# Kernel optimization log

Measured on AMD Instinct MI355X. Metric: run time of the kernel, lower is better.

The kernel has to match this reference:

```python
import jax, jax.numpy as jnp
import numpy as np

N = 100000      # nodes
E = 800000      # edges (avg degree 8)
D_IN = 64
H1 = H2 = H3 = 64
HEADS = 2
D_EDGE = 5
NEG_SLOPE = 0.2  # GATConv leaky_relu slope


def _lin(key, fi, fo):
    kw, kb = jax.random.split(key)
    w = jax.random.normal(kw, (fi, fo), jnp.float32) / np.sqrt(fi)
    b = jax.random.normal(kb, (fo,), jnp.float32) * 0.01
    return w, b


def setup_inputs() -> dict:
    key = jax.random.key(0)
    ks = jax.random.split(key, 16)
    x = jax.random.normal(ks[0], (N, D_IN), jnp.float32)
    edge_index = jax.random.randint(ks[1], (2, E), 0, N, dtype=jnp.int32)
    edge_attr = jax.random.normal(ks[2], (E, D_EDGE), jnp.float32)

    inp = {"x": x, "edge_index": edge_index, "edge_attr": edge_attr}
    dims = [(D_IN, H1), (H1, H2), (H2, H3)]
    for i, (fi, fo) in enumerate(dims, start=1):
        k = jax.random.fold_in(ks[3], i)
        ka, kb, kc = jax.random.split(k, 3)
        inp[f"w_node{i}"], inp[f"b_node{i}"] = _lin(ka, fi, fo)
        inp[f"w_edge{i}"], inp[f"b_edge{i}"] = _lin(kb, D_EDGE, fo)
        inp[f"w_comb{i}"], inp[f"b_comb{i}"] = _lin(kc, 2 * fo, fo)
    # GATConv: shared lin for src/dst, att vectors, bias (concat=False -> size H3)
    kg, ks_, kd, kbias = jax.random.split(ks[4], 4)
    inp["w_gat"] = jax.random.normal(kg, (H3, HEADS * H3), jnp.float32) / np.sqrt(H3)
    inp["att_src"] = jax.random.normal(ks_, (HEADS, H3), jnp.float32) * 0.1
    inp["att_dst"] = jax.random.normal(kd, (HEADS, H3), jnp.float32) * 0.1
    inp["b_gat"] = jax.random.normal(kbias, (H3,), jnp.float32) * 0.01
    return inp


def _edge_conv(h, src, dst, ea, wn, bn, we, be, wc, bc, n):
    # lin_node / lin_edge applied densely, then gather -> concat -> lin -> scatter-add
    hn = h @ wn + bn                       # [N, C]
    ef = ea @ we + be                      # [E, C]
    msg = jnp.concatenate([hn[src], ef], axis=1) @ wc + bc  # [E, C]
    return jax.ops.segment_sum(msg, dst, num_segments=n)


def _gat(h, src, dst, w_gat, att_src, att_dst, b_gat, n):
    g = (h @ w_gat).reshape(n, HEADS, -1)          # [N, H, C]
    a_src = jnp.einsum("nhc,hc->nh", g, att_src)    # [N, H]
    a_dst = jnp.einsum("nhc,hc->nh", g, att_dst)
    alpha = jax.nn.leaky_relu(a_src[src] + a_dst[dst], NEG_SLOPE)  # [E, H]
    # segment softmax over incoming edges of each dst node
    m = jax.ops.segment_max(alpha, dst, num_segments=n)
    alpha = jnp.exp(alpha - m[dst])
    denom = jax.ops.segment_sum(alpha, dst, num_segments=n)
    alpha = alpha / (denom[dst] + 1e-16)
    out = jax.ops.segment_sum(g[src] * alpha[:, :, None], dst, num_segments=n)  # [N,H,C]
    return out.mean(axis=1) + b_gat  # concat=False -> mean over heads, plus bias


def reference(x, edge_index, edge_attr,
              w_node1, b_node1, w_edge1, b_edge1, w_comb1, b_comb1,
              w_node2, b_node2, w_edge2, b_edge2, w_comb2, b_comb2,
              w_node3, b_node3, w_edge3, b_edge3, w_comb3, b_comb3,
              w_gat, att_src, att_dst, b_gat):
    n = x.shape[0]
    src, dst = edge_index[0], edge_index[1]
    h = x
    h = jax.nn.relu(_edge_conv(h, src, dst, edge_attr, w_node1, b_node1, w_edge1, b_edge1, w_comb1, b_comb1, n))
    h = jax.nn.relu(_edge_conv(h, src, dst, edge_attr, w_node2, b_node2, w_edge2, b_edge2, w_comb2, b_comb2, n))
    h = jax.nn.relu(_edge_conv(h, src, dst, edge_attr, w_node3, b_node3, w_edge3, b_edge3, w_comb3, b_comb3, n))
    h = _gat(h, src, dst, w_gat, att_src, att_dst, b_gat, n)
    return h.reshape(-1)  # torch.flatten
```

## Files before the change

kernel.cpp:

```cpp
#include <hip/hip_runtime.h>
#include <hip/hip_fp16.h>
#include <math.h>


#define TPB 256

typedef unsigned int u32;

__device__ inline float2 f16unpack2(u32 u) {
    __half2 h = *reinterpret_cast<__half2*>(&u);
    return __half22float2(h);
}
__device__ inline u32 f16pack2(float lo, float hi) {
    __half2 h = __floats2half2_rn(lo, hi);
    return *reinterpret_cast<u32*>(&h);
}
__device__ inline void fma_f16x8(float* acc, uint4 v, float w) {
    float2 t;
    t = f16unpack2(v.x); acc[0] = fmaf(w, t.x, acc[0]); acc[1] = fmaf(w, t.y, acc[1]);
    t = f16unpack2(v.y); acc[2] = fmaf(w, t.x, acc[2]); acc[3] = fmaf(w, t.y, acc[3]);
    t = f16unpack2(v.z); acc[4] = fmaf(w, t.x, acc[4]); acc[5] = fmaf(w, t.y, acc[5]);
    t = f16unpack2(v.w); acc[6] = fmaf(w, t.x, acc[6]); acc[7] = fmaf(w, t.y, acc[7]);
}
__device__ inline void acc_h16(float4& acc, uint2 v) {
    float2 a = f16unpack2(v.x);
    float2 b = f16unpack2(v.y);
    acc.x += a.x; acc.y += a.y; acc.z += b.x; acc.w += b.y;
}

#define MAC4(acc, a, w0, w1, w2, w3)                                           \
    acc.x = fmaf(a.x, w0.x, acc.x); acc.y = fmaf(a.x, w0.y, acc.y);            \
    acc.z = fmaf(a.x, w0.z, acc.z); acc.w = fmaf(a.x, w0.w, acc.w);            \
    acc.x = fmaf(a.y, w1.x, acc.x); acc.y = fmaf(a.y, w1.y, acc.y);            \
    acc.z = fmaf(a.y, w1.z, acc.z); acc.w = fmaf(a.y, w1.w, acc.w);            \
    acc.x = fmaf(a.z, w2.x, acc.x); acc.y = fmaf(a.z, w2.y, acc.y);            \
    acc.z = fmaf(a.z, w2.z, acc.z); acc.w = fmaf(a.z, w2.w, acc.w);            \
    acc.x = fmaf(a.w, w3.x, acc.x); acc.y = fmaf(a.w, w3.y, acc.y);            \
    acc.z = fmaf(a.w, w3.z, acc.z); acc.w = fmaf(a.w, w3.w, acc.w);

__global__ __launch_bounds__(TPB) void k_hist(const int* __restrict__ dst, int* __restrict__ cnt,
                                              int* __restrict__ rank, int E) {
    int e = blockIdx.x * TPB + threadIdx.x;
    if (e < E) rank[e] = atomicAdd(&cnt[dst[e]], 1);
}

__global__ __launch_bounds__(TPB) void k_scan1(int* __restrict__ data, int* __restrict__ partials, int n) {
    __shared__ int s[TPB];
    int i = blockIdx.x * TPB + threadIdx.x;
    int v = (i < n) ? data[i] : 0;
    s[threadIdx.x] = v;
    __syncthreads();
    for (int off = 1; off < TPB; off <<= 1) {
        int t = (threadIdx.x >= off) ? s[threadIdx.x - off] : 0;
        __syncthreads();
        s[threadIdx.x] += t;
        __syncthreads();
    }
    if (i < n) data[i] = s[threadIdx.x] - v;
    if (threadIdx.x == TPB - 1) partials[blockIdx.x] = s[TPB - 1];
}

__global__ __launch_bounds__(1024) void k_scan2(int* __restrict__ partials, int nb) {
    __shared__ int s[1024];
    int v = (threadIdx.x < nb) ? partials[threadIdx.x] : 0;
    s[threadIdx.x] = v;
    __syncthreads();
    for (int off = 1; off < 1024; off <<= 1) {
        int t = (threadIdx.x >= off) ? s[threadIdx.x - off] : 0;
        __syncthreads();
        s[threadIdx.x] += t;
        __syncthreads();
    }
    if (threadIdx.x < nb) partials[threadIdx.x] = s[threadIdx.x] - v;
}

__global__ __launch_bounds__(TPB) void k_scan3(int* __restrict__ data, const int* __restrict__ partials,
                                               int n, int total) {
    int i = blockIdx.x * TPB + threadIdx.x;
    if (i < n) data[i] += partials[blockIdx.x];
    if (i == 0) data[n] = total;
}

__global__ __launch_bounds__(TPB) void k_scatter(const int* __restrict__ src, const int* __restrict__ dst,
                                                 const int* __restrict__ rank, const int* __restrict__ row_start,
                                                 int2* __restrict__ csr_se, int E) {
    int e = blockIdx.x * TPB + threadIdx.x;
    if (e < E) {
        int idx = row_start[dst[e]] + rank[e];
        csr_se[idx] = make_int2(src[e], e);
    }
}

__global__ __launch_bounds__(TPB) void k_aggB5(const int2* __restrict__ csr_se, const int* __restrict__ row_start,
                                               const float* __restrict__ EA, float* __restrict__ B5, int n) {
    const int node = blockIdx.x * 16 + (threadIdx.x >> 4);
    if (node >= n) return;
    const int lid = threadIdx.x & 15;
    const int beg = row_start[node], end = row_start[node + 1];
    float b0 = 0.f, b1 = 0.f, b2 = 0.f, b3 = 0.f, b4 = 0.f;
    for (int j = beg + lid; j < end; j += 16) {
        int e = csr_se[j].y;
        const float* p = EA + (size_t)e * 5;
        b0 += p[0]; b1 += p[1]; b2 += p[2]; b3 += p[3]; b4 += p[4];
    }
    #pragma unroll
    for (int off = 1; off < 16; off <<= 1) {
        b0 += __shfl_xor(b0, off); b1 += __shfl_xor(b1, off);
        b2 += __shfl_xor(b2, off); b3 += __shfl_xor(b3, off);
        b4 += __shfl_xor(b4, off);
    }
    if (lid == 0) {
        float* bp = B5 + (size_t)node * 5;
        bp[0] = b0; bp[1] = b1; bp[2] = b2; bp[3] = b3; bp[4] = b4;
    }
}

struct CombPtrs {
    const float* wn; const float* bn;
    const float* we; const float* be;
    const float* wc; const float* bc;
    float* W1;
};

__global__ __launch_bounds__(TPB) void k_combine3(CombPtrs p0, CombPtrs p1, CombPtrs p2) {
    CombPtrs P = (blockIdx.x == 0) ? p0 : ((blockIdx.x == 1) ? p1 : p2);
    const float* wn = P.wn; const float* bn = P.bn;
    const float* we = P.we; const float* be = P.be;
    const float* wc = P.wc; const float* bc = P.bc;
    float* W1 = P.W1;
    float* W2 = P.W1 + 4096;
    float* cv = P.W1 + 4416;
    int tid = threadIdx.x;
    for (int idx = tid; idx < 64 * 64; idx += TPB) {
        int i = idx >> 6, j = idx & 63;
        float acc = 0.f;
        #pragma unroll 8
        for (int k = 0; k < 64; k++) acc = fmaf(wn[i * 64 + k], wc[k * 64 + j], acc);
        W1[idx] = acc;
    }
    for (int idx = tid; idx < 5 * 64; idx += TPB) {
        int i = idx >> 6, j = idx & 63;
        float acc = 0.f;
        #pragma unroll 8
        for (int k = 0; k < 64; k++) acc = fmaf(we[i * 64 + k], wc[(64 + k) * 64 + j], acc);
        W2[idx] = acc;
    }
    for (int j = tid; j < 64; j += TPB) {
        float acc = bc[j];
        for (int k = 0; k < 64; k++) {
            acc = fmaf(bn[k], wc[k * 64 + j], acc);
            acc = fmaf(be[k], wc[(64 + k) * 64 + j], acc);
        }
        cv[j] = acc;
    }
}

template <bool IN16, bool OUT16>
__global__ __launch_bounds__(TPB, 6) void k_ec_fused(const void* __restrict__ Hv,
                                                     const int* __restrict__ row_start,
                                                     const int2* __restrict__ csr_se,
                                                     const float* __restrict__ Wfold,
                                                     const float* __restrict__ B5,
                                                     void* __restrict__ OUTv, int n) {
    __shared__ float Alds[64 * 68];
    const float* Hf = (const float*)Hv;
    const u32*   Hh = (const u32*)Hv;
    const int t = threadIdx.x;
    const int base = blockIdx.x * 64;

    const int lane = t & 63;
    const int lid = lane & 15;
    const int gbase = lane & 48;
    const int gid = t >> 4;
    const int c4 = lid * 4;
    const int h2i = lid * 2;
    for (int i = 0; i < 4; i++) {
        int r = gid * 4 + i;
        int node = base + r;
        float4 acc = make_float4(0.f, 0.f, 0.f, 0.f);
        if (node < n) {
            int beg = row_start[node], end = row_start[node + 1];
            for (int chunk = beg; chunk < end; chunk += 16) {
                int cdeg = min(end - chunk, 16);
                int s_l = (chunk + lid < end) ? csr_se[chunk + lid].x : 0;
                int it = 0;
                for (; it + 7 < cdeg; it += 8) {
                    int se0 = __shfl(s_l, gbase + it);
                    int se1 = __shfl(s_l, gbase + it + 1);
                    int se2 = __shfl(s_l, gbase + it + 2);
                    int se3 = __shfl(s_l, gbase + it + 3);
                    int se4 = __shfl(s_l, gbase + it + 4);
                    int se5 = __shfl(s_l, gbase + it + 5);
                    int se6 = __shfl(s_l, gbase + it + 6);
                    int se7 = __shfl(s_l, gbase + it + 7);
                    if (IN16) {
                        uint2 v0 = *(const uint2*)&Hh[(size_t)se0 * 32 + h2i];
                        uint2 v1 = *(const uint2*)&Hh[(size_t)se1 * 32 + h2i];
                        uint2 v2 = *(const uint2*)&Hh[(size_t)se2 * 32 + h2i];
                        uint2 v3 = *(const uint2*)&Hh[(size_t)se3 * 32 + h2i];
                        uint2 v4 = *(const uint2*)&Hh[(size_t)se4 * 32 + h2i];
                        uint2 v5 = *(const uint2*)&Hh[(size_t)se5 * 32 + h2i];
                        uint2 v6 = *(const uint2*)&Hh[(size_t)se6 * 32 + h2i];
                        uint2 v7 = *(const uint2*)&Hh[(size_t)se7 * 32 + h2i];
                        acc_h16(acc, v0); acc_h16(acc, v1); acc_h16(acc, v2); acc_h16(acc, v3);
                        acc_h16(acc, v4); acc_h16(acc, v5); acc_h16(acc, v6); acc_h16(acc, v7);
                    } else {
                        float4 v0 = *(const float4*)&Hf[(size_t)se0 * 64 + c4];
                        float4 v1 = *(const float4*)&Hf[(size_t)se1 * 64 + c4];
                        float4 v2 = *(const float4*)&Hf[(size_t)se2 * 64 + c4];
                        float4 v3 = *(const float4*)&Hf[(size_t)se3 * 64 + c4];
                        float4 v4 = *(const float4*)&Hf[(size_t)se4 * 64 + c4];
                        float4 v5 = *(const float4*)&Hf[(size_t)se5 * 64 + c4];
                        float4 v6 = *(const float4*)&Hf[(size_t)se6 * 64 + c4];
                        float4 v7 = *(const float4*)&Hf[(size_t)se7 * 64 + c4];
                        acc.x += ((v0.x + v1.x) + (v2.x + v3.x)) + ((v4.x + v5.x) + (v6.x + v7.x));
                        acc.y += ((v0.y + v1.y) + (v2.y + v3.y)) + ((v4.y + v5.y) + (v6.y + v7.y));
                        acc.z += ((v0.z + v1.z) + (v2.z + v3.z)) + ((v4.z + v5.z) + (v6.z + v7.z));
                        acc.w += ((v0.w + v1.w) + (v2.w + v3.w)) + ((v4.w + v5.w) + (v6.w + v7.w));
                    }
                }
                for (; it + 3 < cdeg; it += 4) {
                    int se0 = __shfl(s_l, gbase + it);
                    int se1 = __shfl(s_l, gbase + it + 1);
                    int se2 = __shfl(s_l, gbase + it + 2);
                    int se3 = __shfl(s_l, gbase + it + 3);
                    if (IN16) {
                        uint2 v0 = *(const uint2*)&Hh[(size_t)se0 * 32 + h2i];
                        uint2 v1 = *(const uint2*)&Hh[(size_t)se1 * 32 + h2i];
                        uint2 v2 = *(const uint2*)&Hh[(size_t)se2 * 32 + h2i];
                        uint2 v3 = *(const uint2*)&Hh[(size_t)se3 * 32 + h2i];
                        acc_h16(acc, v0); acc_h16(acc, v1); acc_h16(acc, v2); acc_h16(acc, v3);
                    } else {
                        float4 v0 = *(const float4*)&Hf[(size_t)se0 * 64 + c4];
                        float4 v1 = *(const float4*)&Hf[(size_t)se1 * 64 + c4];
                        float4 v2 = *(const float4*)&Hf[(size_t)se2 * 64 + c4];
                        float4 v3 = *(const float4*)&Hf[(size_t)se3 * 64 + c4];
                        acc.x += (v0.x + v1.x) + (v2.x + v3.x);
                        acc.y += (v0.y + v1.y) + (v2.y + v3.y);
                        acc.z += (v0.z + v1.z) + (v2.z + v3.z);
                        acc.w += (v0.w + v1.w) + (v2.w + v3.w);
                    }
                }
                for (; it < cdeg; it++) {
                    int se = __shfl(s_l, gbase + it);
                    if (IN16) {
                        uint2 v = *(const uint2*)&Hh[(size_t)se * 32 + h2i];
                        acc_h16(acc, v);
                    } else {
                        float4 v = *(const float4*)&Hf[(size_t)se * 64 + c4];
                        acc.x += v.x; acc.y += v.y; acc.z += v.z; acc.w += v.w;
                    }
                }
            }
        }
        *(float4*)&Alds[r * 68 + c4] = acc;
    }
    __syncthreads();

    const int r0 = (t >> 4) * 4, c0 = (t & 15) * 4;
    float4 acc0 = make_float4(0.f, 0.f, 0.f, 0.f), acc1 = acc0, acc2 = acc0, acc3 = acc0;
    #pragma unroll 2
    for (int k = 0; k < 64; k += 4) {
        float4 a0 = *(float4*)&Alds[(r0 + 0) * 68 + k];
        float4 a1 = *(float4*)&Alds[(r0 + 1) * 68 + k];
        float4 a2 = *(float4*)&Alds[(r0 + 2) * 68 + k];
        float4 a3 = *(float4*)&Alds[(r0 + 3) * 68 + k];
        float4 w0 = *(const float4*)&Wfold[(k + 0) * 64 + c0];
        float4 w1 = *(const float4*)&Wfold[(k + 1) * 64 + c0];
        float4 w2 = *(const float4*)&Wfold[(k + 2) * 64 + c0];
        float4 w3 = *(const float4*)&Wfold[(k + 3) * 64 + c0];
        MAC4(acc0, a0, w0, w1, w2, w3);
        MAC4(acc1, a1, w0, w1, w2, w3);
        MAC4(acc2, a2, w0, w1, w2, w3);
        MAC4(acc3, a3, w0, w1, w2, w3);
    }
    float4 w2c[5];
    #pragma unroll
    for (int j = 0; j < 5; j++) w2c[j] = *(const float4*)&Wfold[4096 + j * 64 + c0];
    const float4 cv4 = *(const float4*)&Wfold[4416 + c0];
    #define EC_STORE(i, acc)                                                        \
        { int row = base + r0 + i;                                                  \
          if (row < n) {                                                            \
              const float* bp = B5 + (size_t)row * 5;                               \
              float deg = (float)(row_start[row + 1] - row_start[row]);             \
              float4 q;                                                             \
              q.x = deg * cv4.x; q.y = deg * cv4.y;                                 \
              q.z = deg * cv4.z; q.w = deg * cv4.w;                                 \
              for (int j = 0; j < 5; j++) {                                         \
                  float b = bp[j];                                                  \
                  q.x = fmaf(b, w2c[j].x, q.x); q.y = fmaf(b, w2c[j].y, q.y);       \
                  q.z = fmaf(b, w2c[j].z, q.z); q.w = fmaf(b, w2c[j].w, q.w);       \
              }                                                                     \
              float4 r4;                                                            \
              r4.x = fmaxf(acc.x + q.x, 0.f); r4.y = fmaxf(acc.y + q.y, 0.f);       \
              r4.z = fmaxf(acc.z + q.z, 0.f); r4.w = fmaxf(acc.w + q.w, 0.f);       \
              if (OUT16) {                                                          \
                  u32* O = (u32*)OUTv;                                              \
                  uint2 g;                                                          \
                  g.x = f16pack2(r4.x, r4.y); g.y = f16pack2(r4.z, r4.w);           \
                  *(uint2*)&O[(size_t)row * 32 + (c0 >> 1)] = g;                    \
              } else {                                                              \
                  float* O = (float*)OUTv;                                          \
                  *(float4*)&O[(size_t)row * 64 + c0] = r4;                         \
              } } }
    EC_STORE(0, acc0) EC_STORE(1, acc1) EC_STORE(2, acc2) EC_STORE(3, acc3)
    #undef EC_STORE
}

__global__ __launch_bounds__(TPB) void k_gemm_gat(const u32* __restrict__ Hh, const float* __restrict__ W,
                                                  const float* __restrict__ att_src, const float* __restrict__ att_dst,
                                                  u32* __restrict__ Gh, float* __restrict__ asrc,
                                                  float* __restrict__ adst, int n) {
    __shared__ float Alds[64 * 68];
    __shared__ float Wlds[64 * 132];
    const int t = threadIdx.x;
    const int base = blockIdx.x * 64;
    {
        int r16 = t >> 4, cc = (t & 15) * 4;
        #pragma unroll
        for (int rep = 0; rep < 4; rep++) {
            int r = rep * 16 + r16;
            int row = base + r;
            float4 v = make_float4(0.f, 0.f, 0.f, 0.f);
            if (row < n) {
                uint2 h = *(const uint2*)&Hh[(size_t)row * 32 + (cc >> 1)];
                float2 a = f16unpack2(h.x), b = f16unpack2(h.y);
                v = make_float4(a.x, a.y, b.x, b.y);
            }
            *(float4*)&Alds[r * 68 + cc] = v;
        }
        #pragma unroll
        for (int rep = 0; rep < 8; rep++) {
            int idx4 = (rep * 256 + t) * 4;
            int r = idx4 >> 7, c = idx4 & 127;
            *(float4*)&Wlds[r * 132 + c] = *(const float4*)&W[r * 128 + c];
        }
    }
    __syncthreads();

    const int r0 = (t >> 4) * 4, c0 = (t & 15) * 4;
    float4 p00 = make_float4(0.f, 0.f, 0.f, 0.f), p01 = p00, p02 = p00, p03 = p00;
    float4 p10 = p00, p11 = p00, p12 = p00, p13 = p00;
    #pragma unroll 2
    for (int k = 0; k < 64; k += 4) {
        float4 a0 = *(float4*)&Alds[(r0 + 0) * 68 + k];
        float4 a1 = *(float4*)&Alds[(r0 + 1) * 68 + k];
        float4 a2 = *(float4*)&Alds[(r0 + 2) * 68 + k];
        float4 a3 = *(float4*)&Alds[(r0 + 3) * 68 + k];
        float4 u0 = *(float4*)&Wlds[(k + 0) * 132 + c0];
        float4 u1 = *(float4*)&Wlds[(k + 1) * 132 + c0];
        float4 u2 = *(float4*)&Wlds[(k + 2) * 132 + c0];
        float4 u3 = *(float4*)&Wlds[(k + 3) * 132 + c0];
        MAC4(p00, a0, u0, u1, u2, u3);
        MAC4(p01, a1, u0, u1, u2, u3);
        MAC4(p02, a2, u0, u1, u2, u3);
        MAC4(p03, a3, u0, u1, u2, u3);
        float4 v0 = *(float4*)&Wlds[(k + 0) * 132 + 64 + c0];
        float4 v1 = *(float4*)&Wlds[(k + 1) * 132 + 64 + c0];
        float4 v2 = *(float4*)&Wlds[(k + 2) * 132 + 64 + c0];
        float4 v3 = *(float4*)&Wlds[(k + 3) * 132 + 64 + c0];
        MAC4(p10, a0, v0, v1, v2, v3);
        MAC4(p11, a1, v0, v1, v2, v3);
        MAC4(p12, a2, v0, v1, v2, v3);
        MAC4(p13, a3, v0, v1, v2, v3);
    }
    const float4 as0 = *(const float4*)&att_src[c0];
    const float4 as1 = *(const float4*)&att_src[64 + c0];
    const float4 ad0 = *(const float4*)&att_dst[c0];
    const float4 ad1 = *(const float4*)&att_dst[64 + c0];
    #define DOT4(a, b) (a.x * b.x + a.y * b.y + a.z * b.z + a.w * b.w)
    #define GAT_ROW(i, h0, h1)                                                      \
        { int row = base + r0 + i;                                                  \
          float s0 = DOT4(h0, as0), s1 = DOT4(h1, as1);                             \
          float d0 = DOT4(h0, ad0), d1 = DOT4(h1, ad1);                             \
          s0 += __shfl_xor(s0, 1); s1 += __shfl_xor(s1, 1);                         \
          d0 += __shfl_xor(d0, 1); d1 += __shfl_xor(d1, 1);                         \
          s0 += __shfl_xor(s0, 2); s1 += __shfl_xor(s1, 2);                         \
          d0 += __shfl_xor(d0, 2); d1 += __shfl_xor(d1, 2);                         \
          s0 += __shfl_xor(s0, 4); s1 += __shfl_xor(s1, 4);                         \
          d0 += __shfl_xor(d0, 4); d1 += __shfl_xor(d1, 4);                         \
          s0 += __shfl_xor(s0, 8); s1 += __shfl_xor(s1, 8);                         \
          d0 += __shfl_xor(d0, 8); d1 += __shfl_xor(d1, 8);                         \
          if (row < n) {                                                            \
              uint2 g0; g0.x = f16pack2(h0.x, h0.y); g0.y = f16pack2(h0.z, h0.w);   \
              uint2 g1; g1.x = f16pack2(h1.x, h1.y); g1.y = f16pack2(h1.z, h1.w);   \
              *(uint2*)&Gh[(size_t)row * 64 + (c0 >> 1)] = g0;                      \
              *(uint2*)&Gh[(size_t)row * 64 + 32 + (c0 >> 1)] = g1;                 \
              if ((t & 15) == 0) {                                                  \
                  float2 sv; sv.x = s0; sv.y = s1;                                  \
                  float2 dv; dv.x = d0; dv.y = d1;                                  \
                  *(float2*)&asrc[(size_t)row * 2] = sv;                            \
                  *(float2*)&adst[(size_t)row * 2] = dv; } } }
    GAT_ROW(0, p00, p10) GAT_ROW(1, p01, p11) GAT_ROW(2, p02, p12) GAT_ROW(3, p03, p13)
    #undef GAT_ROW
    #undef DOT4
}

__global__ __launch_bounds__(TPB) void k_gat_agg(const u32* __restrict__ Gh, const int* __restrict__ row_start,
                                                 const int2* __restrict__ csr_se, const float* __restrict__ asrc,
                                                 const float* __restrict__ adst, const float* __restrict__ bgat,
                                                 float* __restrict__ OUT, int n) {
    const int node = blockIdx.x * 16 + (threadIdx.x >> 4);
    if (node >= n) return;
    const int lane = threadIdx.x & 63;
    const int lid = lane & 15;
    const int gbase = lane & 48;
    const int head = lid >> 3;
    const int u4 = lid * 4;
    const int beg = row_start[node], end = row_start[node + 1];
    const float2 adv = *(const float2*)&adst[(size_t)node * 2];
    float m0 = -INFINITY, m1 = -INFINITY, d0 = 0.f, d1 = 0.f;
    float A[8] = {0.f, 0.f, 0.f, 0.f, 0.f, 0.f, 0.f, 0.f};
    for (int chunk = beg; chunk < end; chunk += 16) {
        int cdeg = min(end - chunk, 16);
        bool valid = (lid < cdeg);
        int s_l = valid ? csr_se[chunk + lid].x : 0;
        float al0 = -INFINITY, al1 = -INFINITY;
        if (valid) {
            float2 av = *(const float2*)&asrc[(size_t)s_l * 2];
            float t0 = av.x + adv.x, t1 = av.y + adv.y;
            al0 = (t0 > 0.f) ? t0 : 0.2f * t0;
            al1 = (t1 > 0.f) ? t1 : 0.2f * t1;
        }
        float cm0 = al0, cm1 = al1;
        #pragma unroll
        for (int off = 1; off < 16; off <<= 1) {
            cm0 = fmaxf(cm0, __shfl_xor(cm0, off));
            cm1 = fmaxf(cm1, __shfl_xor(cm1, off));
        }
        float nm0 = fmaxf(m0, cm0), nm1 = fmaxf(m1, cm1);
        float sc0 = __expf(m0 - nm0), sc1 = __expf(m1 - nm1);
        float w0 = valid ? __expf(al0 - nm0) : 0.f;
        float w1 = valid ? __expf(al1 - nm1) : 0.f;
        float cd0 = w0, cd1 = w1;
        #pragma unroll
        for (int off = 1; off < 16; off <<= 1) {
            cd0 += __shfl_xor(cd0, off);
            cd1 += __shfl_xor(cd1, off);
        }
        d0 = d0 * sc0 + cd0;
        d1 = d1 * sc1 + cd1;
        float scsel = head ? sc1 : sc0;
        #pragma unroll
        for (int j = 0; j < 8; j++) A[j] *= scsel;
        m0 = nm0; m1 = nm1;
        int it = 0;
        for (; it + 3 < cdeg; it += 4) {
            int sa = __shfl(s_l, gbase + it);
            int sb = __shfl(s_l, gbase + it + 1);
            int sc = __shfl(s_l, gbase + it + 2);
            int sd = __shfl(s_l, gbase + it + 3);
            float w0a = __shfl(w0, gbase + it),     w1a = __shfl(w1, gbase + it);
            float w0b = __shfl(w0, gbase + it + 1), w1b = __shfl(w1, gbase + it + 1);
            float w0c = __shfl(w0, gbase + it + 2), w1c = __shfl(w1, gbase + it + 2);
            float w0d = __shfl(w0, gbase + it + 3), w1d = __shfl(w1, gbase + it + 3);
            float wa = head ? w1a : w0a;
            float wb = head ? w1b : w0b;
            float wc = head ? w1c : w0c;
            float wd = head ? w1d : w0d;
            uint4 va = *(const uint4*)&Gh[(size_t)sa * 64 + u4];
            uint4 vb = *(const uint4*)&Gh[(size_t)sb * 64 + u4];
            uint4 vc = *(const uint4*)&Gh[(size_t)sc * 64 + u4];
            uint4 vd = *(const uint4*)&Gh[(size_t)sd * 64 + u4];
            fma_f16x8(A, va, wa);
            fma_f16x8(A, vb, wb);
            fma_f16x8(A, vc, wc);
            fma_f16x8(A, vd, wd);
        }
        for (; it + 1 < cdeg; it += 2) {
            int sa = __shfl(s_l, gbase + it);
            int sb = __shfl(s_l, gbase + it + 1);
            float w0a = __shfl(w0, gbase + it),     w1a = __shfl(w1, gbase + it);
            float w0b = __shfl(w0, gbase + it + 1), w1b = __shfl(w1, gbase + it + 1);
            float wa = head ? w1a : w0a;
            float wb = head ? w1b : w0b;
            uint4 va = *(const uint4*)&Gh[(size_t)sa * 64 + u4];
            uint4 vb = *(const uint4*)&Gh[(size_t)sb * 64 + u4];
            fma_f16x8(A, va, wa);
            fma_f16x8(A, vb, wb);
        }
        if (it < cdeg) {
            int sa = __shfl(s_l, gbase + it);
            float w0a = __shfl(w0, gbase + it), w1a = __shfl(w1, gbase + it);
            float wa = head ? w1a : w0a;
            uint4 va = *(const uint4*)&Gh[(size_t)sa * 64 + u4];
            fma_f16x8(A, va, wa);
        }
    }
    float rh = 0.5f / ((head ? d1 : d0) + 1e-16f);
    #pragma unroll
    for (int j = 0; j < 8; j++) {
        A[j] *= rh;
        A[j] += __shfl_xor(A[j], 8);
    }
    if (head == 0) {
        int cb = (lid & 7) * 8;
        const float4 bg0 = *(const float4*)&bgat[cb];
        const float4 bg1 = *(const float4*)&bgat[cb + 4];
        float4 o0; o0.x = A[0] + bg0.x; o0.y = A[1] + bg0.y; o0.z = A[2] + bg0.z; o0.w = A[3] + bg0.w;
        float4 o1; o1.x = A[4] + bg1.x; o1.y = A[5] + bg1.y; o1.z = A[6] + bg1.z; o1.w = A[7] + bg1.w;
        float* op = &OUT[(size_t)node * 64 + cb];
        *(float4*)op = o0;
        *(float4*)(op + 4) = o1;
    }
}

extern "C" void kernel_launch(void* const* d_in, const int* in_sizes, int n_in,
                              void* d_out, int out_size, void* d_ws, size_t ws_size,
                              hipStream_t stream) {
    const float* x   = (const float*)d_in[0];
    const int*   ei  = (const int*)d_in[1];
    const float* ea  = (const float*)d_in[2];
    const int N = in_sizes[0] / 64;
    const int E = in_sizes[1] / 2;
    const int* src = ei;
    const int* dst = ei + E;

    const float* wn[3] = {(const float*)d_in[3],  (const float*)d_in[9],  (const float*)d_in[15]};
    const float* bn[3] = {(const float*)d_in[4],  (const float*)d_in[10], (const float*)d_in[16]};
    const float* we[3] = {(const float*)d_in[5],  (const float*)d_in[11], (const float*)d_in[17]};
    const float* be[3] = {(const float*)d_in[6],  (const float*)d_in[12], (const float*)d_in[18]};
    const float* wc[3] = {(const float*)d_in[7],  (const float*)d_in[13], (const float*)d_in[19]};
    const float* bc[3] = {(const float*)d_in[8],  (const float*)d_in[14], (const float*)d_in[20]};
    const float* wgat    = (const float*)d_in[21];
    const float* att_src = (const float*)d_in[22];
    const float* att_dst = (const float*)d_in[23];
    const float* bgat    = (const float*)d_in[24];

    char* ws = (char*)d_ws;
    size_t off = 0;
    auto alloc = [&](size_t bytes) -> void* {
        void* p = ws + off;
        off = (off + bytes + 255) & ~(size_t)255;
        return p;
    };
    int*   row_start = (int*)alloc((size_t)(N + 1) * 4);
    int*   partials  = (int*)alloc(1024 * 4);
    int*   rank      = (int*)alloc((size_t)E * 4);
    int2*  csr_se    = (int2*)alloc((size_t)E * 8);
    float* Wc        = (float*)alloc((size_t)3 * 4480 * 4);
    float* B5        = (float*)alloc((size_t)N * 5 * 4);
    u32*   bufH0     = (u32*)alloc((size_t)N * 64 * 2);
    u32*   bufH1     = (u32*)alloc((size_t)N * 64 * 2);
    u32*   Gh        = (u32*)alloc((size_t)N * 64 * 4);
    float* asrc      = (float*)alloc((size_t)N * 2 * 4);
    float* adst      = (float*)alloc((size_t)N * 2 * 4);
    float* out = (float*)d_out;

    const int nbN = (N + TPB - 1) / TPB;
    const int nbE = (E + TPB - 1) / TPB;
    const int grpBlocks = (N + 15) / 16;
    const int tiles = (N + 63) / 64;

    CombPtrs p0 = {wn[0], bn[0], we[0], be[0], wc[0], bc[0], Wc};
    CombPtrs p1 = {wn[1], bn[1], we[1], be[1], wc[1], bc[1], Wc + 4480};
    CombPtrs p2 = {wn[2], bn[2], we[2], be[2], wc[2], bc[2], Wc + 2 * 4480};
    k_combine3<<<3, TPB, 0, stream>>>(p0, p1, p2);

    hipMemsetAsync(row_start, 0, (size_t)N * 4, stream);
    k_hist<<<nbE, TPB, 0, stream>>>(dst, row_start, rank, E);
    k_scan1<<<nbN, TPB, 0, stream>>>(row_start, partials, N);
    k_scan2<<<1, 1024, 0, stream>>>(partials, nbN);
    k_scan3<<<nbN, TPB, 0, stream>>>(row_start, partials, N, E);
    k_scatter<<<nbE, TPB, 0, stream>>>(src, dst, rank, row_start, csr_se, E);
    k_aggB5<<<grpBlocks, TPB, 0, stream>>>(csr_se, row_start, ea, B5, N);

    k_ec_fused<false, true><<<tiles, TPB, 0, stream>>>(x,     row_start, csr_se, Wc,            B5, bufH0, N);
    k_ec_fused<true,  true><<<tiles, TPB, 0, stream>>>(bufH0, row_start, csr_se, Wc + 4480,     B5, bufH1, N);
    k_ec_fused<true,  true><<<tiles, TPB, 0, stream>>>(bufH1, row_start, csr_se, Wc + 2 * 4480, B5, bufH0, N);

    k_gemm_gat<<<tiles, TPB, 0, stream>>>(bufH0, wgat, att_src, att_dst, Gh, asrc, adst, N);
    k_gat_agg<<<grpBlocks, TPB, 0, stream>>>(Gh, row_start, csr_se, asrc, adst, bgat, out, N);
}
```

Before: 414.8 us.

## Sort tile edges by source and aggregate via LDS atomics in edge-conv

Adds a per-64-node-tile bitonic sort of incoming edges keyed by source node, packing source index and local row into one int. The edge-conv kernels then walk the tile's edges flat, 64 at a time, gathering neighbour features and accumulating them into the shared tile with LDS atomicAdd. This removes the per-node degree imbalance and shuffle-based loops, and aims for better gather locality. In exchange it adds a sort kernel, an extra edge array, and per-element LDS atomics that may contend. The packed key assumes the source index shifted left by six still fits in an int, which holds for N=100000.

```diff
diff --git a/kernel.cpp b/kernel.cpp
--- a/kernel.cpp
+++ b/kernel.cpp
@@ -21,11 +21,6 @@
     t = f16unpack2(v.y); acc[2] = fmaf(w, t.x, acc[2]); acc[3] = fmaf(w, t.y, acc[3]);
     t = f16unpack2(v.z); acc[4] = fmaf(w, t.x, acc[4]); acc[5] = fmaf(w, t.y, acc[5]);
     t = f16unpack2(v.w); acc[6] = fmaf(w, t.x, acc[6]); acc[7] = fmaf(w, t.y, acc[7]);
-}
-__device__ inline void acc_h16(float4& acc, uint2 v) {
-    float2 a = f16unpack2(v.x);
-    float2 b = f16unpack2(v.y);
-    acc.x += a.x; acc.y += a.y; acc.z += b.x; acc.w += b.y;
 }
 
 #define MAC4(acc, a, w0, w1, w2, w3)                                           \
@@ -112,6 +107,50 @@
     if (lid == 0) {
         float* bp = B5 + (size_t)node * 5;
         bp[0] = b0; bp[1] = b1; bp[2] = b2; bp[3] = b3; bp[4] = b4;
+    }
+}
+
+__global__ __launch_bounds__(TPB) void k_tilesort(const int2* __restrict__ csr_se,
+                                                  const int* __restrict__ row_start,
+                                                  int* __restrict__ tile_edges, int n) {
+    __shared__ int keys[1024];
+    __shared__ int roff[65];
+    const int t = threadIdx.x;
+    const int base = blockIdx.x * 64;
+    const int nb = min(64, n - base);
+    if (t <= nb) roff[t] = row_start[base + t];
+    __syncthreads();
+    const int beg = roff[0], end = roff[nb];
+    const int m = end - beg;
+    if (m <= 1024) {
+        for (int i = t; i < 1024; i += TPB) keys[i] = 0x7FFFFFFF;
+        __syncthreads();
+        if (t < nb) {
+            int a = roff[t], b = roff[t + 1];
+            for (int j = a; j < b; j++) keys[j - beg] = (csr_se[j].x << 6) | t;
+        }
+        __syncthreads();
+        for (int kk = 2; kk <= 1024; kk <<= 1) {
+            for (int jj = kk >> 1; jj > 0; jj >>= 1) {
+                for (int i = t; i < 1024; i += TPB) {
+                    int p = i ^ jj;
+                    if (p > i) {
+                        int a = keys[i], b = keys[p];
+                        bool up = ((i & kk) == 0);
+                        if ((a > b) == up) { keys[i] = b; keys[p] = a; }
+                    }
+                }
+                __syncthreads();
+            }
+        }
+        for (int i = t; i < m; i += TPB) tile_edges[beg + i] = keys[i];
+    } else {
+        for (int i = t; i < m; i += TPB) {
+            int j = beg + i;
+            int lo = 0, hi = nb;
+            while (hi - lo > 1) { int mid = (lo + hi) >> 1; if (roff[mid] <= j) lo = mid; else hi = mid; }
+            tile_edges[j] = (csr_se[j].x << 6) | lo;
+        }
     }
 }
 
@@ -158,7 +197,7 @@
 template <bool IN16, bool OUT16>
 __global__ __launch_bounds__(TPB, 6) void k_ec_fused(const void* __restrict__ Hv,
                                                      const int* __restrict__ row_start,
-                                                     const int2* __restrict__ csr_se,
+                                                     const int* __restrict__ tile_edges,
                                                      const float* __restrict__ Wfold,
                                                      const float* __restrict__ B5,
                                                      void* __restrict__ OUTv, int n) {
@@ -168,92 +207,50 @@
     const int t = threadIdx.x;
     const int base = blockIdx.x * 64;
 
-    const int lane = t & 63;
-    const int lid = lane & 15;
-    const int gbase = lane & 48;
-    const int gid = t >> 4;
-    const int c4 = lid * 4;
-    const int h2i = lid * 2;
-    for (int i = 0; i < 4; i++) {
-        int r = gid * 4 + i;
-        int node = base + r;
-        float4 acc = make_float4(0.f, 0.f, 0.f, 0.f);
-        if (node < n) {
-            int beg = row_start[node], end = row_start[node + 1];
-            for (int chunk = beg; chunk < end; chunk += 16) {
-                int cdeg = min(end - chunk, 16);
-                int s_l = (chunk + lid < end) ? csr_se[chunk + lid].x : 0;
-                int it = 0;
-                for (; it + 7 < cdeg; it += 8) {
-                    int se0 = __shfl(s_l, gbase + it);
-                    int se1 = __shfl(s_l, gbase + it + 1);
-                    int se2 = __shfl(s_l, gbase + it + 2);
-                    int se3 = __shfl(s_l, gbase + it + 3);
-                    int se4 = __shfl(s_l, gbase + it + 4);
-                    int se5 = __shfl(s_l, gbase + it + 5);
-                    int se6 = __shfl(s_l, gbase + it + 6);
-                    int se7 = __shfl(s_l, gbase + it + 7);
-                    if (IN16) {
-                        uint2 v0 = *(const uint2*)&Hh[(size_t)se0 * 32 + h2i];
-                        uint2 v1 = *(const uint2*)&Hh[(size_t)se1 * 32 + h2i];
-                        uint2 v2 = *(const uint2*)&Hh[(size_t)se2 * 32 + h2i];
-                        uint2 v3 = *(const uint2*)&Hh[(size_t)se3 * 32 + h2i];
-                        uint2 v4 = *(const uint2*)&Hh[(size_t)se4 * 32 + h2i];
-                        uint2 v5 = *(const uint2*)&Hh[(size_t)se5 * 32 + h2i];
-                        uint2 v6 = *(const uint2*)&Hh[(size_t)se6 * 32 + h2i];
-                        uint2 v7 = *(const uint2*)&Hh[(size_t)se7 * 32 + h2i];
-                        acc_h16(acc, v0); acc_h16(acc, v1); acc_h16(acc, v2); acc_h16(acc, v3);
-                        acc_h16(acc, v4); acc_h16(acc, v5); acc_h16(acc, v6); acc_h16(acc, v7);
-                    } else {
-                        float4 v0 = *(const float4*)&Hf[(size_t)se0 * 64 + c4];
-                        float4 v1 = *(const float4*)&Hf[(size_t)se1 * 64 + c4];
-                        float4 v2 = *(const float4*)&Hf[(size_t)se2 * 64 + c4];
-                        float4 v3 = *(const float4*)&Hf[(size_t)se3 * 64 + c4];
-                        float4 v4 = *(const float4*)&Hf[(size_t)se4 * 64 + c4];
-                        float4 v5 = *(const float4*)&Hf[(size_t)se5 * 64 + c4];
-                        float4 v6 = *(const float4*)&Hf[(size_t)se6 * 64 + c4];
-                        float4 v7 = *(const float4*)&Hf[(size_t)se7 * 64 + c4];
-                        acc.x += ((v0.x + v1.x) + (v2.x + v3.x)) + ((v4.x + v5.x) + (v6.x + v7.x));
-                        acc.y += ((v0.y + v1.y) + (v2.y + v3.y)) + ((v4.y + v5.y) + (v6.y + v7.y));
-                        acc.z += ((v0.z + v1.z) + (v2.z + v3.z)) + ((v4.z + v5.z) + (v6.z + v7.z));
-                        acc.w += ((v0.w + v1.w) + (v2.w + v3.w)) + ((v4.w + v5.w) + (v6.w + v7.w));
-                    }
-                }
-                for (; it + 3 < cdeg; it += 4) {
-                    int se0 = __shfl(s_l, gbase + it);
-                    int se1 = __shfl(s_l, gbase + it + 1);
-                    int se2 = __shfl(s_l, gbase + it + 2);
-                    int se3 = __shfl(s_l, gbase + it + 3);
-                    if (IN16) {
-                        uint2 v0 = *(const uint2*)&Hh[(size_t)se0 * 32 + h2i];
-                        uint2 v1 = *(const uint2*)&Hh[(size_t)se1 * 32 + h2i];
-                        uint2 v2 = *(const uint2*)&Hh[(size_t)se2 * 32 + h2i];
-                        uint2 v3 = *(const uint2*)&Hh[(size_t)se3 * 32 + h2i];
-                        acc_h16(acc, v0); acc_h16(acc, v1); acc_h16(acc, v2); acc_h16(acc, v3);
-                    } else {
-                        float4 v0 = *(const float4*)&Hf[(size_t)se0 * 64 + c4];
-                        float4 v1 = *(const float4*)&Hf[(size_t)se1 * 64 + c4];
-                        float4 v2 = *(const float4*)&Hf[(size_t)se2 * 64 + c4];
-                        float4 v3 = *(const float4*)&Hf[(size_t)se3 * 64 + c4];
-                        acc.x += (v0.x + v1.x) + (v2.x + v3.x);
-                        acc.y += (v0.y + v1.y) + (v2.y + v3.y);
-                        acc.z += (v0.z + v1.z) + (v2.z + v3.z);
-                        acc.w += (v0.w + v1.w) + (v2.w + v3.w);
-                    }
-                }
-                for (; it < cdeg; it++) {
-                    int se = __shfl(s_l, gbase + it);
-                    if (IN16) {
-                        uint2 v = *(const uint2*)&Hh[(size_t)se * 32 + h2i];
-                        acc_h16(acc, v);
-                    } else {
-                        float4 v = *(const float4*)&Hf[(size_t)se * 64 + c4];
-                        acc.x += v.x; acc.y += v.y; acc.z += v.z; acc.w += v.w;
-                    }
+    for (int i = t; i < 64 * 68; i += TPB) Alds[i] = 0.f;
+
+    const int g   = t >> 4;
+    const int lid = t & 15;
+    const int col4 = ((lid + g) & 15) * 4;
+    const int hb = min(base + 64, n);
+    const int beg = row_start[base], end = row_start[hb];
+    __syncthreads();
+
+    for (int e0 = beg; e0 < end; e0 += 64) {
+        int key[4];
+        #pragma unroll
+        for (int k = 0; k < 4; k++) {
+            int e = e0 + g + k * 16;
+            key[k] = (e < end) ? tile_edges[e] : -1;
+        }
+        if (IN16) {
+            uint2 hv[4];
+            #pragma unroll
+            for (int k = 0; k < 4; k++)
+                if (key[k] >= 0) hv[k] = *(const uint2*)&Hh[(size_t)(key[k] >> 6) * 32 + (col4 >> 1)];
+            #pragma unroll
+            for (int k = 0; k < 4; k++) {
+                if (key[k] >= 0) {
+                    float* ap = &Alds[(key[k] & 63) * 68 + col4];
+                    float2 a = f16unpack2(hv[k].x), b = f16unpack2(hv[k].y);
+                    atomicAdd(ap + 0, a.x); atomicAdd(ap + 1, a.y);
+                    atomicAdd(ap + 2, b.x); atomicAdd(ap + 3, b.y);
                 }
             }
-        }
-        *(float4*)&Alds[r * 68 + c4] = acc;
+        } else {
+            float4 hv[4];
+            #pragma unroll
+            for (int k = 0; k < 4; k++)
+                if (key[k] >= 0) hv[k] = *(const float4*)&Hf[(size_t)(key[k] >> 6) * 64 + col4];
+            #pragma unroll
+            for (int k = 0; k < 4; k++) {
+                if (key[k] >= 0) {
+                    float* ap = &Alds[(key[k] & 63) * 68 + col4];
+                    atomicAdd(ap + 0, hv[k].x); atomicAdd(ap + 1, hv[k].y);
+                    atomicAdd(ap + 2, hv[k].z); atomicAdd(ap + 3, hv[k].w);
+                }
+            }
+        }
     }
     __syncthreads();
 
@@ -296,9 +293,9 @@
               r4.z = fmaxf(acc.z + q.z, 0.f); r4.w = fmaxf(acc.w + q.w, 0.f);       \
               if (OUT16) {                                                          \
                   u32* O = (u32*)OUTv;                                              \
-                  uint2 g;                                                          \
-                  g.x = f16pack2(r4.x, r4.y); g.y = f16pack2(r4.z, r4.w);           \
-                  *(uint2*)&O[(size_t)row * 32 + (c0 >> 1)] = g;                    \
+                  uint2 gg;                                                         \
+                  gg.x = f16pack2(r4.x, r4.y); gg.y = f16pack2(r4.z, r4.w);         \
+                  *(uint2*)&O[(size_t)row * 32 + (c0 >> 1)] = gg;                   \
               } else {                                                              \
                   float* O = (float*)OUTv;                                          \
                   *(float4*)&O[(size_t)row * 64 + c0] = r4;                         \
@@ -534,17 +531,18 @@
         off = (off + bytes + 255) & ~(size_t)255;
         return p;
     };
-    int*   row_start = (int*)alloc((size_t)(N + 1) * 4);
-    int*   partials  = (int*)alloc(1024 * 4);
-    int*   rank      = (int*)alloc((size_t)E * 4);
-    int2*  csr_se    = (int2*)alloc((size_t)E * 8);
-    float* Wc        = (float*)alloc((size_t)3 * 4480 * 4);
-    float* B5        = (float*)alloc((size_t)N * 5 * 4);
-    u32*   bufH0     = (u32*)alloc((size_t)N * 64 * 2);
-    u32*   bufH1     = (u32*)alloc((size_t)N * 64 * 2);
-    u32*   Gh        = (u32*)alloc((size_t)N * 64 * 4);
-    float* asrc      = (float*)alloc((size_t)N * 2 * 4);
-    float* adst      = (float*)alloc((size_t)N * 2 * 4);
+    int*   row_start  = (int*)alloc((size_t)(N + 1) * 4);
+    int*   partials   = (int*)alloc(1024 * 4);
+    int*   rank       = (int*)alloc((size_t)E * 4);
+    int2*  csr_se     = (int2*)alloc((size_t)E * 8);
+    int*   tile_edges = (int*)alloc((size_t)E * 4);
+    float* Wc         = (float*)alloc((size_t)3 * 4480 * 4);
+    float* B5         = (float*)alloc((size_t)N * 5 * 4);
+    u32*   bufH0      = (u32*)alloc((size_t)N * 64 * 2);
+    u32*   bufH1      = (u32*)alloc((size_t)N * 64 * 2);
+    u32*   Gh         = (u32*)alloc((size_t)N * 64 * 4);
+    float* asrc       = (float*)alloc((size_t)N * 2 * 4);
+    float* adst       = (float*)alloc((size_t)N * 2 * 4);
     float* out = (float*)d_out;
 
     const int nbN = (N + TPB - 1) / TPB;
@@ -564,10 +562,11 @@
     k_scan3<<<nbN, TPB, 0, stream>>>(row_start, partials, N, E);
     k_scatter<<<nbE, TPB, 0, stream>>>(src, dst, rank, row_start, csr_se, E);
     k_aggB5<<<grpBlocks, TPB, 0, stream>>>(csr_se, row_start, ea, B5, N);
-
-    k_ec_fused<false, true><<<tiles, TPB, 0, stream>>>(x,     row_start, csr_se, Wc,            B5, bufH0, N);
-    k_ec_fused<true,  true><<<tiles, TPB, 0, stream>>>(bufH0, row_start, csr_se, Wc + 4480,     B5, bufH1, N);
-    k_ec_fused<true,  true><<<tiles, TPB, 0, stream>>>(bufH1, row_start, csr_se, Wc + 2 * 4480, B5, bufH0, N);
+    k_tilesort<<<tiles, TPB, 0, stream>>>(csr_se, row_start, tile_edges, N);
+
+    k_ec_fused<false, true><<<tiles, TPB, 0, stream>>>(x,     row_start, tile_edges, Wc,            B5, bufH0, N);
+    k_ec_fused<true,  true><<<tiles, TPB, 0, stream>>>(bufH0, row_start, tile_edges, Wc + 4480,     B5, bufH1, N);
+    k_ec_fused<true,  true><<<tiles, TPB, 0, stream>>>(bufH1, row_start, tile_edges, Wc + 2 * 4480, B5, bufH0, N);
 
     k_gemm_gat<<<tiles, TPB, 0, stream>>>(bufH0, wgat, att_src, att_dst, Gh, asrc, adst, N);
     k_gat_agg<<<grpBlocks, TPB, 0, stream>>>(Gh, row_start, csr_se, asrc, adst, bgat, out, N);
```

Measured after the change: 1.252 ms. +201.8%, slower.

## Fuse GAT projection into last edge-conv kernel and drop scan2 launch

Applied to the files above, without the earlier changes.

The third edge-conv layer now keeps its ReLU output tile in LDS and immediately runs the GAT linear projection and attention-score dot products. This removes the separate k_gemm_gat kernel along with its fp16 round trip of the hidden state through global memory. The single-block k_scan2 is also removed: each k_scan3 block now sums the preceding block partials itself. The occupancy hint on k_ec_fused is lowered from 6 to 4, and the GAT weights are read from global memory rather than staged in LDS, which may increase register pressure and cache traffic.

```diff
diff --git a/kernel.cpp b/kernel.cpp
--- a/kernel.cpp
+++ b/kernel.cpp
@@ -60,24 +60,19 @@
     if (threadIdx.x == TPB - 1) partials[blockIdx.x] = s[TPB - 1];
 }
 
-__global__ __launch_bounds__(1024) void k_scan2(int* __restrict__ partials, int nb) {
-    __shared__ int s[1024];
-    int v = (threadIdx.x < nb) ? partials[threadIdx.x] : 0;
-    s[threadIdx.x] = v;
-    __syncthreads();
-    for (int off = 1; off < 1024; off <<= 1) {
-        int t = (threadIdx.x >= off) ? s[threadIdx.x - off] : 0;
-        __syncthreads();
-        s[threadIdx.x] += t;
-        __syncthreads();
-    }
-    if (threadIdx.x < nb) partials[threadIdx.x] = s[threadIdx.x] - v;
-}
-
 __global__ __launch_bounds__(TPB) void k_scan3(int* __restrict__ data, const int* __restrict__ partials,
                                                int n, int total) {
-    int i = blockIdx.x * TPB + threadIdx.x;
-    if (i < n) data[i] += partials[blockIdx.x];
+    const int bid = blockIdx.x;
+    int s = 0;
+    for (int j = threadIdx.x; j < bid; j += TPB) s += partials[j];
+    #pragma unroll
+    for (int off = 32; off > 0; off >>= 1) s += __shfl_down(s, off);
+    __shared__ int ws[4];
+    if ((threadIdx.x & 63) == 0) ws[threadIdx.x >> 6] = s;
+    __syncthreads();
+    int pre = ws[0] + ws[1] + ws[2] + ws[3];
+    int i = bid * TPB + threadIdx.x;
+    if (i < n) data[i] += pre;
     if (i == 0) data[n] = total;
 }
 
@@ -155,13 +150,19 @@
     }
 }
 
-template <bool IN16, bool OUT16>
-__global__ __launch_bounds__(TPB, 6) void k_ec_fused(const void* __restrict__ Hv,
+template <bool IN16, bool OUT16, bool GAT>
+__global__ __launch_bounds__(TPB, 4) void k_ec_fused(const void* __restrict__ Hv,
                                                      const int* __restrict__ row_start,
                                                      const int2* __restrict__ csr_se,
                                                      const float* __restrict__ Wfold,
                                                      const float* __restrict__ B5,
-                                                     void* __restrict__ OUTv, int n) {
+                                                     void* __restrict__ OUTv, int n,
+                                                     const float* __restrict__ Wg,
+                                                     const float* __restrict__ att_src,
+                                                     const float* __restrict__ att_dst,
+                                                     u32* __restrict__ Gh,
+                                                     float* __restrict__ asrc,
+                                                     float* __restrict__ adst) {
     __shared__ float Alds[64 * 68];
     const float* Hf = (const float*)Hv;
     const u32*   Hh = (const u32*)Hv;
@@ -278,6 +279,9 @@
     #pragma unroll
     for (int j = 0; j < 5; j++) w2c[j] = *(const float4*)&Wfold[4096 + j * 64 + c0];
     const float4 cv4 = *(const float4*)&Wfold[4416 + c0];
+
+    if (GAT) __syncthreads();
+
     #define EC_STORE(i, acc)                                                        \
         { int row = base + r0 + i;                                                  \
           if (row < n) {                                                            \
@@ -294,106 +298,78 @@
               float4 r4;                                                            \
               r4.x = fmaxf(acc.x + q.x, 0.f); r4.y = fmaxf(acc.y + q.y, 0.f);       \
               r4.z = fmaxf(acc.z + q.z, 0.f); r4.w = fmaxf(acc.w + q.w, 0.f);       \
-              if (OUT16) {                                                          \
+              if (GAT) {                                                            \
+                  *(float4*)&Alds[(r0 + i) * 68 + c0] = r4;                         \
+              } else if (OUT16) {                                                   \
                   u32* O = (u32*)OUTv;                                              \
-                  uint2 g;                                                          \
-                  g.x = f16pack2(r4.x, r4.y); g.y = f16pack2(r4.z, r4.w);           \
-                  *(uint2*)&O[(size_t)row * 32 + (c0 >> 1)] = g;                    \
+                  uint2 gg;                                                         \
+                  gg.x = f16pack2(r4.x, r4.y); gg.y = f16pack2(r4.z, r4.w);         \
+                  *(uint2*)&O[(size_t)row * 32 + (c0 >> 1)] = gg;                   \
               } else {                                                              \
                   float* O = (float*)OUTv;                                          \
                   *(float4*)&O[(size_t)row * 64 + c0] = r4;                         \
               } } }
     EC_STORE(0, acc0) EC_STORE(1, acc1) EC_STORE(2, acc2) EC_STORE(3, acc3)
     #undef EC_STORE
-}
-
-__global__ __launch_bounds__(TPB) void k_gemm_gat(const u32* __restrict__ Hh, const float* __restrict__ W,
-                                                  const float* __restrict__ att_src, const float* __restrict__ att_dst,
-                                                  u32* __restrict__ Gh, float* __restrict__ asrc,
-                                                  float* __restrict__ adst, int n) {
-    __shared__ float Alds[64 * 68];
-    __shared__ float Wlds[64 * 132];
-    const int t = threadIdx.x;
-    const int base = blockIdx.x * 64;
-    {
-        int r16 = t >> 4, cc = (t & 15) * 4;
-        #pragma unroll
-        for (int rep = 0; rep < 4; rep++) {
-            int r = rep * 16 + r16;
-            int row = base + r;
-            float4 v = make_float4(0.f, 0.f, 0.f, 0.f);
-            if (row < n) {
-                uint2 h = *(const uint2*)&Hh[(size_t)row * 32 + (cc >> 1)];
-                float2 a = f16unpack2(h.x), b = f16unpack2(h.y);
-                v = make_float4(a.x, a.y, b.x, b.y);
-            }
-            *(float4*)&Alds[r * 68 + cc] = v;
-        }
-        #pragma unroll
-        for (int rep = 0; rep < 8; rep++) {
-            int idx4 = (rep * 256 + t) * 4;
-            int r = idx4 >> 7, c = idx4 & 127;
-            *(float4*)&Wlds[r * 132 + c] = *(const float4*)&W[r * 128 + c];
-        }
-    }
-    __syncthreads();
-
-    const int r0 = (t >> 4) * 4, c0 = (t & 15) * 4;
-    float4 p00 = make_float4(0.f, 0.f, 0.f, 0.f), p01 = p00, p02 = p00, p03 = p00;
-    float4 p10 = p00, p11 = p00, p12 = p00, p13 = p00;
-    #pragma unroll 2
-    for (int k = 0; k < 64; k += 4) {
-        float4 a0 = *(float4*)&Alds[(r0 + 0) * 68 + k];
-        float4 a1 = *(float4*)&Alds[(r0 + 1) * 68 + k];
-        float4 a2 = *(float4*)&Alds[(r0 + 2) * 68 + k];
-        float4 a3 = *(float4*)&Alds[(r0 + 3) * 68 + k];
-        float4 u0 = *(float4*)&Wlds[(k + 0) * 132 + c0];
-        float4 u1 = *(float4*)&Wlds[(k + 1) * 132 + c0];
-        float4 u2 = *(float4*)&Wlds[(k + 2) * 132 + c0];
-        float4 u3 = *(float4*)&Wlds[(k + 3) * 132 + c0];
-        MAC4(p00, a0, u0, u1, u2, u3);
-        MAC4(p01, a1, u0, u1, u2, u3);
-        MAC4(p02, a2, u0, u1, u2, u3);
-        MAC4(p03, a3, u0, u1, u2, u3);
-        float4 v0 = *(float4*)&Wlds[(k + 0) * 132 + 64 + c0];
-        float4 v1 = *(float4*)&Wlds[(k + 1) * 132 + 64 + c0];
-        float4 v2 = *(float4*)&Wlds[(k + 2) * 132 + 64 + c0];
-        float4 v3 = *(float4*)&Wlds[(k + 3) * 132 + 64 + c0];
-        MAC4(p10, a0, v0, v1, v2, v3);
-        MAC4(p11, a1, v0, v1, v2, v3);
-        MAC4(p12, a2, v0, v1, v2, v3);
-        MAC4(p13, a3, v0, v1, v2, v3);
-    }
-    const float4 as0 = *(const float4*)&att_src[c0];
-    const float4 as1 = *(const float4*)&att_src[64 + c0];
-    const float4 ad0 = *(const float4*)&att_dst[c0];
-    const float4 ad1 = *(const float4*)&att_dst[64 + c0];
-    #define DOT4(a, b) (a.x * b.x + a.y * b.y + a.z * b.z + a.w * b.w)
-    #define GAT_ROW(i, h0, h1)                                                      \
-        { int row = base + r0 + i;                                                  \
-          float s0 = DOT4(h0, as0), s1 = DOT4(h1, as1);                             \
-          float d0 = DOT4(h0, ad0), d1 = DOT4(h1, ad1);                             \
-          s0 += __shfl_xor(s0, 1); s1 += __shfl_xor(s1, 1);                         \
-          d0 += __shfl_xor(d0, 1); d1 += __shfl_xor(d1, 1);                         \
-          s0 += __shfl_xor(s0, 2); s1 += __shfl_xor(s1, 2);                         \
-          d0 += __shfl_xor(d0, 2); d1 += __shfl_xor(d1, 2);                         \
-          s0 += __shfl_xor(s0, 4); s1 += __shfl_xor(s1, 4);                         \
-          d0 += __shfl_xor(d0, 4); d1 += __shfl_xor(d1, 4);                         \
-          s0 += __shfl_xor(s0, 8); s1 += __shfl_xor(s1, 8);                         \
-          d0 += __shfl_xor(d0, 8); d1 += __shfl_xor(d1, 8);                         \
-          if (row < n) {                                                            \
-              uint2 g0; g0.x = f16pack2(h0.x, h0.y); g0.y = f16pack2(h0.z, h0.w);   \
-              uint2 g1; g1.x = f16pack2(h1.x, h1.y); g1.y = f16pack2(h1.z, h1.w);   \
-              *(uint2*)&Gh[(size_t)row * 64 + (c0 >> 1)] = g0;                      \
-              *(uint2*)&Gh[(size_t)row * 64 + 32 + (c0 >> 1)] = g1;                 \
-              if ((t & 15) == 0) {                                                  \
-                  float2 sv; sv.x = s0; sv.y = s1;                                  \
-                  float2 dv; dv.x = d0; dv.y = d1;                                  \
-                  *(float2*)&asrc[(size_t)row * 2] = sv;                            \
-                  *(float2*)&adst[(size_t)row * 2] = dv; } } }
-    GAT_ROW(0, p00, p10) GAT_ROW(1, p01, p11) GAT_ROW(2, p02, p12) GAT_ROW(3, p03, p13)
-    #undef GAT_ROW
-    #undef DOT4
+
+    if (GAT) {
+        __syncthreads();
+        float4 p00 = make_float4(0.f, 0.f, 0.f, 0.f), p01 = p00, p02 = p00, p03 = p00;
+        float4 p10 = p00, p11 = p00, p12 = p00, p13 = p00;
+        #pragma unroll 2
+        for (int k = 0; k < 64; k += 4) {
+            float4 a0 = *(float4*)&Alds[(r0 + 0) * 68 + k];
+            float4 a1 = *(float4*)&Alds[(r0 + 1) * 68 + k];
+            float4 a2 = *(float4*)&Alds[(r0 + 2) * 68 + k];
+            float4 a3 = *(float4*)&Alds[(r0 + 3) * 68 + k];
+            float4 u0 = *(const float4*)&Wg[(k + 0) * 128 + c0];
+            float4 u1 = *(const float4*)&Wg[(k + 1) * 128 + c0];
+            float4 u2 = *(const float4*)&Wg[(k + 2) * 128 + c0];
+            float4 u3 = *(const float4*)&Wg[(k + 3) * 128 + c0];
+            MAC4(p00, a0, u0, u1, u2, u3);
+            MAC4(p01, a1, u0, u1, u2, u3);
+            MAC4(p02, a2, u0, u1, u2, u3);
+            MAC4(p03, a3, u0, u1, u2, u3);
+            float4 v0 = *(const float4*)&Wg[(k + 0) * 128 + 64 + c0];
+            float4 v1 = *(const float4*)&Wg[(k + 1) * 128 + 64 + c0];
+            float4 v2 = *(const float4*)&Wg[(k + 2) * 128 + 64 + c0];
+            float4 v3 = *(const float4*)&Wg[(k + 3) * 128 + 64 + c0];
+            MAC4(p10, a0, v0, v1, v2, v3);
+            MAC4(p11, a1, v0, v1, v2, v3);
+            MAC4(p12, a2, v0, v1, v2, v3);
+            MAC4(p13, a3, v0, v1, v2, v3);
+        }
+        const float4 as0 = *(const float4*)&att_src[c0];
+        const float4 as1 = *(const float4*)&att_src[64 + c0];
+        const float4 ad0 = *(const float4*)&att_dst[c0];
+        const float4 ad1 = *(const float4*)&att_dst[64 + c0];
+        #define DOT4(a, b) (a.x * b.x + a.y * b.y + a.z * b.z + a.w * b.w)
+        #define GAT_ROW(i, h0, h1)                                                      \
+            { int row = base + r0 + i;                                                  \
+              float s0 = DOT4(h0, as0), s1 = DOT4(h1, as1);                             \
+              float d0 = DOT4(h0, ad0), d1 = DOT4(h1, ad1);                             \
+              s0 += __shfl_xor(s0, 1); s1 += __shfl_xor(s1, 1);                         \
+              d0 += __shfl_xor(d0, 1); d1 += __shfl_xor(d1, 1);                         \
+              s0 += __shfl_xor(s0, 2); s1 += __shfl_xor(s1, 2);                         \
+              d0 += __shfl_xor(d0, 2); d1 += __shfl_xor(d1, 2);                         \
+              s0 += __shfl_xor(s0, 4); s1 += __shfl_xor(s1, 4);                         \
+              d0 += __shfl_xor(d0, 4); d1 += __shfl_xor(d1, 4);                         \
+              s0 += __shfl_xor(s0, 8); s1 += __shfl_xor(s1, 8);                         \
+              d0 += __shfl_xor(d0, 8); d1 += __shfl_xor(d1, 8);                         \
+              if (row < n) {                                                            \
+                  uint2 g0; g0.x = f16pack2(h0.x, h0.y); g0.y = f16pack2(h0.z, h0.w);   \
+                  uint2 g1; g1.x = f16pack2(h1.x, h1.y); g1.y = f16pack2(h1.z, h1.w);   \
+                  *(uint2*)&Gh[(size_t)row * 64 + (c0 >> 1)] = g0;                      \
+                  *(uint2*)&Gh[(size_t)row * 64 + 32 + (c0 >> 1)] = g1;                 \
+                  if ((t & 15) == 0) {                                                  \
+                      float2 sv; sv.x = s0; sv.y = s1;                                  \
+                      float2 dv; dv.x = d0; dv.y = d1;                                  \
+                      *(float2*)&asrc[(size_t)row * 2] = sv;                            \
+                      *(float2*)&adst[(size_t)row * 2] = dv; } } }
+        GAT_ROW(0, p00, p10) GAT_ROW(1, p01, p11) GAT_ROW(2, p02, p12) GAT_ROW(3, p03, p13)
+        #undef GAT_ROW
+        #undef DOT4
+    }
 }
 
 __global__ __launch_bounds__(TPB) void k_gat_agg(const u32* __restrict__ Gh, const int* __restrict__ row_start,
@@ -560,15 +536,19 @@
     hipMemsetAsync(row_start, 0, (size_t)N * 4, stream);
     k_hist<<<nbE, TPB, 0, stream>>>(dst, row_start, rank, E);
     k_scan1<<<nbN, TPB, 0, stream>>>(row_start, partials, N);
-    k_scan2<<<1, 1024, 0, stream>>>(partials, nbN);
     k_scan3<<<nbN, TPB, 0, stream>>>(row_start, partials, N, E);
     k_scatter<<<nbE, TPB, 0, stream>>>(src, dst, rank, row_start, csr_se, E);
     k_aggB5<<<grpBlocks, TPB, 0, stream>>>(csr_se, row_start, ea, B5, N);
 
-    k_ec_fused<false, true><<<tiles, TPB, 0, stream>>>(x,     row_start, csr_se, Wc,            B5, bufH0, N);
-    k_ec_fused<true,  true><<<tiles, TPB, 0, stream>>>(bufH0, row_start, csr_se, Wc + 4480,     B5, bufH1, N);
-    k_ec_fused<true,  true><<<tiles, TPB, 0, stream>>>(bufH1, row_start, csr_se, Wc + 2 * 4480, B5, bufH0, N);
-
-    k_gemm_gat<<<tiles, TPB, 0, stream>>>(bufH0, wgat, att_src, att_dst, Gh, asrc, adst, N);
+    k_ec_fused<false, true, false><<<tiles, TPB, 0, stream>>>(
+        x,     row_start, csr_se, Wc,            B5, bufH0, N,
+        nullptr, nullptr, nullptr, nullptr, nullptr, nullptr);
+    k_ec_fused<true,  true, false><<<tiles, TPB, 0, stream>>>(
+        bufH0, row_start, csr_se, Wc + 4480,     B5, bufH1, N,
+        nullptr, nullptr, nullptr, nullptr, nullptr, nullptr);
+    k_ec_fused<true,  true, true><<<tiles, TPB, 0, stream>>>(
+        bufH1, row_start, csr_se, Wc + 2 * 4480, B5, nullptr, N,
+        wgat, att_src, att_dst, Gh, asrc, adst);
+
     k_gat_agg<<<grpBlocks, TPB, 0, stream>>>(Gh, row_start, csr_se, asrc, adst, bgat, out, N);
 }
```

After: 415.8 us. Within noise of the previous version (+0.3%).
